# Kernel optimization log

Measured on AMD Instinct MI355X. Metric: run time of the kernel, lower is better.

Reference implementation:

```python
import jax, jax.numpy as jnp
import numpy as np

ENT_TYPES = 9
INNER_DIM = 64
BIG_NEG = 1e12


def _rope_tables(seq_len, dim, dtype):
    # sinusoidal_position_embedding: interleaved [sin, cos] of pos * 10000^(-2i/d)
    pos = jnp.arange(seq_len, dtype=jnp.float32)[:, None]            # [S,1]
    inv_freq = jnp.power(10000.0, -2.0 * jnp.arange(dim // 2, dtype=jnp.float32) / dim)
    ang = pos * inv_freq                                             # [S,D/2]
    emb = jnp.stack([jnp.sin(ang), jnp.cos(ang)], axis=-1).reshape(seq_len, dim)  # [S,D]
    cos_pos = jnp.repeat(emb[:, 1::2], 2, axis=-1).astype(dtype)     # [S,D]
    sin_pos = jnp.repeat(emb[:, ::2], 2, axis=-1).astype(dtype)      # [S,D]
    return cos_pos, sin_pos


def _rotate_half(x):
    # stack([-x[...,1::2], x[...,::2]], -1).reshape(x.shape)
    return jnp.stack([-x[..., 1::2], x[..., ::2]], axis=-1).reshape(x.shape)


def setup_inputs() -> dict:
    key = jax.random.key(0)
    k1, k2 = jax.random.split(key)
    B, S, H = 16, 512, 1024
    last_hidden_state = jax.random.normal(k1, (B, S, H), dtype=jnp.float32)
    padding_mask = jnp.ones((B, S), dtype=jnp.float32)
    W = jax.random.normal(k2, (H, ENT_TYPES * INNER_DIM * 2), dtype=jnp.float32) * (1.0 / np.sqrt(H))
    b = jnp.zeros((ENT_TYPES * INNER_DIM * 2,), dtype=jnp.float32)
    return {"last_hidden_state": last_hidden_state, "padding_mask": padding_mask, "W": W, "b": b}


def reference(last_hidden_state, padding_mask, W, b):
    B, S, _ = last_hidden_state.shape
    H, D = ENT_TYPES, INNER_DIM
    out = last_hidden_state @ W + b                 # [B,S,H*2D]
    out = out.reshape(B, S, H, 2 * D)
    qw, kw = out[..., :D], out[..., D:]             # [B,S,H,D]

    cos_pos, sin_pos = _rope_tables(S, D, qw.dtype)  # [S,D]
    cos_pos = cos_pos[None, :, None, :]
    sin_pos = sin_pos[None, :, None, :]
    qw = qw * cos_pos + _rotate_half(qw) * sin_pos
    kw = kw * cos_pos + _rotate_half(kw) * sin_pos

    logits = jnp.einsum('bmhd,bnhd->bhmn', qw, kw)   # [B,H,S,S]
    pad = padding_mask[:, None, None, :]             # mask over key dim
    logits = logits * pad - (1.0 - pad) * BIG_NEG
    tril = jnp.tril(jnp.ones((S, S), dtype=logits.dtype), -1)
    logits = logits - tril * BIG_NEG
    return logits / jnp.sqrt(jnp.asarray(D, dtype=logits.dtype))
```

## Files before the change

kernel.cpp:

```cpp
#include <hip/hip_runtime.h>

#define EN 9
#define DD 64
#define SS 512
#define NB 16
#define HH 1024
#define NOUT 1152

typedef short bf16x8 __attribute__((ext_vector_type(8)));
typedef short short4v __attribute__((ext_vector_type(4)));
typedef float f32x4 __attribute__((ext_vector_type(4)));

#define GPTR(p) ((const __attribute__((address_space(1))) void*)(p))
#define LPTR(p) ((__attribute__((address_space(3))) void*)(p))

__device__ inline unsigned short f2bf(float f) {
  unsigned int u = __float_as_uint(f);
  return (unsigned short)((u + 0x7FFFu + ((u >> 16) & 1u)) >> 16);
}

__global__ __launch_bounds__(256) void prep_kernel(
    const float* __restrict__ W, const float* __restrict__ X,
    unsigned short* __restrict__ Wt, unsigned short* __restrict__ Xb,
    float* __restrict__ ctab, float* __restrict__ stab) {
  if (blockIdx.x < 288u) {
    __shared__ float t[64][65];
    const int k0 = (blockIdx.x / 18) * 64;
    const int n0 = (blockIdx.x % 18) * 64;
    const int r = threadIdx.x >> 6;
    const int c = threadIdx.x & 63;
#pragma unroll
    for (int i = 0; i < 16; ++i) {
      const int kk = (i << 2) + r;
      t[kk][c] = W[(size_t)(k0 + kk) * NOUT + n0 + c];
    }
    __syncthreads();
#pragma unroll
    for (int i = 0; i < 16; ++i) {
      const int nn = (i << 2) + r;
      Wt[(size_t)(n0 + nn) * HH + k0 + c] = f2bf(t[c][nn]);
    }
  } else if (blockIdx.x < 304u) {
    const int bt = blockIdx.x - 288;
#pragma unroll
    for (int j = 0; j < 4; ++j) {
      const int id = bt * 1024 + j * 256 + threadIdx.x;
      const int s = id >> 5, i = id & 31;
      const float freq = expf(-(float)(2 * i) * (9.210340371976184f / 64.0f));
      const float ang = (float)s * freq;
      ctab[id] = cosf(ang);
      stab[id] = sinf(ang);
    }
  } else {
    const int bt = blockIdx.x - 304;
    const size_t base = (size_t)bt * 4096;
#pragma unroll
    for (int j = 0; j < 4; ++j) {
      const size_t idx = base + (size_t)((j << 8) + threadIdx.x) * 4;
      const float4 v = *(const float4*)(X + idx);
      short4v s4;
      s4[0] = (short)f2bf(v.x);
      s4[1] = (short)f2bf(v.y);
      s4[2] = (short)f2bf(v.z);
      s4[3] = (short)f2bf(v.w);
      *(short4v*)(Xb + idx) = s4;
    }
  }
}

__global__ __launch_bounds__(256, 2) void proj_rope_kernel(
    const unsigned short* __restrict__ Xb,
    const unsigned short* __restrict__ Wt, const float* __restrict__ bias,
    const float* __restrict__ ctab, const float* __restrict__ stab,
    unsigned short* __restrict__ QK) {
  __shared__ __align__(16) unsigned char sm[65536];
  const int tid = threadIdx.x;
  const int lane = tid & 63;
  const int wid = tid >> 6;
  const int wr = wid >> 1, wc = wid & 1;
  const int f = blockIdx.x;
  const int wkr = (f & 7) * 72 + (f >> 3);
  const int m0 = (wkr / 9) << 7;
  const int n0 = (wkr % 9) << 7;

  const int r_st = tid >> 3;
  const int cl_st = tid & 7;

  f32x4 acc[4][4];
#pragma unroll
  for (int i = 0; i < 4; ++i)
#pragma unroll
    for (int j = 0; j < 4; ++j) acc[i][j] = (f32x4){0.f, 0.f, 0.f, 0.f};

#define STAGE(BUF, KT)                                                        \
  {                                                                           \
    const int kt_ = (KT);                                                     \
    unsigned char* dst_ = sm + (BUF)*32768;                                   \
    _Pragma("unroll") for (int it = 0; it < 4; ++it) {                        \
      const int r_ = (it << 5) + r_st;                                        \
      const int cs_ = cl_st ^ (r_ & 7);                                       \
      __builtin_amdgcn_global_load_lds(                                       \
          GPTR(Xb + (size_t)(m0 + r_) * HH + kt_ + (cs_ << 3)),               \
          LPTR(dst_ + (((it << 8) + (wid << 6)) << 4)), 16, 0, 0);            \
      __builtin_amdgcn_global_load_lds(                                       \
          GPTR(Wt + (size_t)(n0 + r_) * HH + kt_ + (cs_ << 3)),               \
          LPTR(dst_ + 16384 + (((it << 8) + (wid << 6)) << 4)), 16, 0, 0);    \
    }                                                                         \
  }

#define COMPUTE(BUF)                                                          \
  {                                                                           \
    const unsigned char* smc_ = sm + (BUF)*32768;                             \
    _Pragma("unroll") for (int kb = 0; kb < 2; ++kb) {                        \
      bf16x8 af[4], bfr[4];                                                   \
      const int ca = (kb << 2) + (lane >> 4);                                 \
      _Pragma("unroll") for (int i = 0; i < 4; ++i) {                         \
        const int ra = (wr << 6) + (i << 4) + (lane & 15);                    \
        af[i] = *(const bf16x8*)(smc_ + (ra << 7) + ((ca ^ (ra & 7)) << 4));  \
        const int rb = (wc << 6) + (i << 4) + (lane & 15);                    \
        bfr[i] =                                                              \
            *(const bf16x8*)(smc_ + 16384 + (rb << 7) + ((ca ^ (rb & 7))      \
                                                         << 4));              \
      }                                                                       \
      _Pragma("unroll") for (int mi = 0; mi < 4; ++mi)                        \
          _Pragma("unroll") for (int ni = 0; ni < 4; ++ni) acc[mi][ni] =      \
          __builtin_amdgcn_mfma_f32_16x16x32_bf16(af[mi], bfr[ni],            \
                                                  acc[mi][ni], 0, 0, 0);      \
    }                                                                         \
  }

  STAGE(0, 0)
#pragma unroll 1
  for (int t = 0; t < 15; ++t) {
    STAGE((t + 1) & 1, (t + 1) << 6)
    asm volatile("s_waitcnt vmcnt(8)" ::: "memory");
    __builtin_amdgcn_s_barrier();
    __builtin_amdgcn_sched_barrier(0);
    COMPUTE(t & 1)
    __builtin_amdgcn_sched_barrier(0);
    __builtin_amdgcn_s_barrier();
  }
  asm volatile("s_waitcnt vmcnt(0)" ::: "memory");
  __builtin_amdgcn_s_barrier();
  __builtin_amdgcn_sched_barrier(0);
  COMPUTE(1)

#pragma unroll
  for (int mi = 0; mi < 4; ++mi) {
#pragma unroll
    for (int ni = 0; ni < 4; ++ni) {
      const int n = n0 + (wc << 6) + (ni << 4) + (lane & 15);
      const float bn = bias[n];
      const int h = n >> 7, t = (n >> 6) & 1, d = n & 63;
      const int i2 = d >> 1;
      const bool ev = (d & 1) == 0;
#pragma unroll
      for (int r = 0; r < 4; ++r) {
        const int m = m0 + (wr << 6) + (mi << 4) + ((lane >> 4) << 2) + r;
        const int s = m & (SS - 1);
        const int bb = m >> 9;
        const float v = acc[mi][ni][r] + bn;
        const float p = __shfl_xor(v, 1);
        const float cs = ctab[(s << 5) + i2];
        const float sn = stab[(s << 5) + i2];
        const float o = ev ? (v * cs - p * sn) : (v * cs + p * sn);
        QK[((((size_t)bb * EN + h) * 2 + t) * SS + s) * DD + d] = f2bf(o);
      }
    }
  }
}

__global__ __launch_bounds__(256, 4) void logits_kernel(
    const unsigned short* __restrict__ QK, const float* __restrict__ pmask,
    float* __restrict__ out) {
  __shared__ __align__(16) unsigned char sm[32768];
  const int tid = threadIdx.x;
  const int lane = tid & 63;
  const int wid = tid >> 6;
  const int wr = wid >> 1, wc = wid & 1;
  const int f = blockIdx.x;
  const int wkr = (f & 7) * 288 + (f >> 3);
  const int bh = wkr >> 4;
  const int bb = bh / EN;
  const int tm = (wkr >> 2) & 3, tn = wkr & 3;
  const int mq0 = tm << 7, nk0 = tn << 7;
  const unsigned short* Qb = QK + (size_t)bh * 2 * SS * DD;
  const unsigned short* Kb = Qb + SS * DD;

#pragma unroll
  for (int it = 0; it < 4; ++it) {
    const int q = it * 256 + tid;
    const int r = q >> 3, cl = q & 7;
    const int cs = cl ^ (r & 7);
    __builtin_amdgcn_global_load_lds(
        GPTR(Qb + (size_t)(mq0 + r) * DD + (cs << 3)),
        LPTR(sm + ((it * 256 + wid * 64) << 4)), 16, 0, 0);
    __builtin_amdgcn_global_load_lds(
        GPTR(Kb + (size_t)(nk0 + r) * DD + (cs << 3)),
        LPTR(sm + 16384 + ((it * 256 + wid * 64) << 4)), 16, 0, 0);
  }
  __syncthreads();

  f32x4 acc[4][4];
#pragma unroll
  for (int i = 0; i < 4; ++i)
#pragma unroll
    for (int j = 0; j < 4; ++j) acc[i][j] = (f32x4){0.f, 0.f, 0.f, 0.f};

#pragma unroll
  for (int kb = 0; kb < 2; ++kb) {
    bf16x8 af[4], bfr[4];
    const int ca = (kb << 2) + (lane >> 4);
#pragma unroll
    for (int i = 0; i < 4; ++i) {
      const int ra = (wr << 6) + (i << 4) + (lane & 15);
      af[i] = *(const bf16x8*)(sm + (ra << 7) + ((ca ^ (ra & 7)) << 4));
      const int rb = (wc << 6) + (i << 4) + (lane & 15);
      bfr[i] =
          *(const bf16x8*)(sm + 16384 + (rb << 7) + ((ca ^ (rb & 7)) << 4));
    }
#pragma unroll
    for (int mi = 0; mi < 4; ++mi)
#pragma unroll
      for (int ni = 0; ni < 4; ++ni)
        acc[mi][ni] = __builtin_amdgcn_mfma_f32_16x16x32_bf16(
            af[mi], bfr[ni], acc[mi][ni], 0, 0, 0);
  }

#pragma unroll
  for (int mi = 0; mi < 4; ++mi) {
#pragma unroll
    for (int ni = 0; ni < 4; ++ni) {
      const int n = nk0 + (wc << 6) + (ni << 4) + (lane & 15);
      const float pd = pmask[bb * SS + n];
      const float sub = (1.0f - pd) * 1e12f;
#pragma unroll
      for (int r = 0; r < 4; ++r) {
        const int m = mq0 + (wr << 6) + (mi << 4) + ((lane >> 4) << 2) + r;
        float v = acc[mi][ni][r] * pd - sub;
        if (m > n) v -= 1e12f;
        out[((size_t)bh * SS + m) * SS + n] = v * 0.125f;
      }
    }
  }
}

extern "C" void kernel_launch(void* const* d_in, const int* in_sizes, int n_in,
                              void* d_out, int out_size, void* d_ws,
                              size_t ws_size, hipStream_t stream) {
  const float* X = (const float*)d_in[0];
  const float* pm = (const float*)d_in[1];
  const float* W = (const float*)d_in[2];
  const float* bias = (const float*)d_in[3];
  float* out = (float*)d_out;
  unsigned char* ws = (unsigned char*)d_ws;
  unsigned short* QK = (unsigned short*)ws;
  unsigned short* Wt = (unsigned short*)(ws + 18874368);
  float* ctab = (float*)(ws + 21233664);
  float* stab = (float*)(ws + 21299200);
  unsigned short* Xb = (unsigned short*)(ws + 21364736);

  prep_kernel<<<dim3(2352), dim3(256), 0, stream>>>(W, X, Wt, Xb, ctab, stab);
  proj_rope_kernel<<<dim3(576), dim3(256), 0, stream>>>(Xb, Wt, bias, ctab,
                                                        stab, QK);
  logits_kernel<<<dim3(2304), dim3(256), 0, stream>>>(QK, pm, out);
}
```

Before: 71.84 us.

## Switch projection GEMM inputs from bf16 to fp8 with pre-swizzled layout

The prep kernel now converts X and W to fp8 (packed via cvt_pk_fp8) instead of bf16 and writes them in an XOR-swizzled layout. The projection GEMM then streams half the bytes, uses fp8 MFMA instructions, halves its LDS footprint to allow four blocks per CU, and raises wave priority during compute. The aim is to cut memory traffic and conversion cost in the prep and GEMM stages. It adds substantial precision loss in the projection, with a risk of accuracy tolerance failures.

```diff
diff --git a/kernel.cpp b/kernel.cpp
--- a/kernel.cpp
+++ b/kernel.cpp
@@ -3,12 +3,9 @@
 #define EN 9
 #define DD 64
 #define SS 512
-#define NB 16
 #define HH 1024
 #define NOUT 1152
 
-typedef short bf16x8 __attribute__((ext_vector_type(8)));
-typedef short short4v __attribute__((ext_vector_type(4)));
 typedef float f32x4 __attribute__((ext_vector_type(4)));
 
 #define GPTR(p) ((const __attribute__((address_space(1))) void*)(p))
@@ -19,9 +16,15 @@
   return (unsigned short)((u + 0x7FFFu + ((u >> 16) & 1u)) >> 16);
 }
 
+__device__ inline int pk4_fp8(float a, float b, float c, float d) {
+  int v = __builtin_amdgcn_cvt_pk_fp8_f32(a, b, 0, false);
+  v = __builtin_amdgcn_cvt_pk_fp8_f32(c, d, v, true);
+  return v;
+}
+
 __global__ __launch_bounds__(256) void prep_kernel(
     const float* __restrict__ W, const float* __restrict__ X,
-    unsigned short* __restrict__ Wt, unsigned short* __restrict__ Xb,
+    unsigned char* __restrict__ Wf8, unsigned char* __restrict__ Xf8,
     float* __restrict__ ctab, float* __restrict__ stab) {
   if (blockIdx.x < 288u) {
     __shared__ float t[64][65];
@@ -36,9 +39,18 @@
     }
     __syncthreads();
 #pragma unroll
-    for (int i = 0; i < 16; ++i) {
-      const int nn = (i << 2) + r;
-      Wt[(size_t)(n0 + nn) * HH + k0 + c] = f2bf(t[c][nn]);
+    for (int i = 0; i < 2; ++i) {
+      const int p = (i << 8) + threadIdx.x;
+      const int n = p >> 3, cc = p & 7;
+      const int kk = cc << 3;
+      const int lo = pk4_fp8(t[kk][n], t[kk + 1][n], t[kk + 2][n], t[kk + 3][n]);
+      const int hi =
+          pk4_fp8(t[kk + 4][n], t[kk + 5][n], t[kk + 6][n], t[kk + 7][n]);
+      const int gn = n0 + n;
+      int2 v;
+      v.x = lo;
+      v.y = hi;
+      *(int2*)(Wf8 + (size_t)gn * HH + k0 + ((cc ^ (gn & 7)) << 3)) = v;
     }
   } else if (blockIdx.x < 304u) {
     const int bt = blockIdx.x - 288;
@@ -53,27 +65,26 @@
     }
   } else {
     const int bt = blockIdx.x - 304;
-    const size_t base = (size_t)bt * 4096;
 #pragma unroll
     for (int j = 0; j < 4; ++j) {
-      const size_t idx = base + (size_t)((j << 8) + threadIdx.x) * 4;
-      const float4 v = *(const float4*)(X + idx);
-      short4v s4;
-      s4[0] = (short)f2bf(v.x);
-      s4[1] = (short)f2bf(v.y);
-      s4[2] = (short)f2bf(v.z);
-      s4[3] = (short)f2bf(v.w);
-      *(short4v*)(Xb + idx) = s4;
-    }
-  }
-}
-
-__global__ __launch_bounds__(256, 2) void proj_rope_kernel(
-    const unsigned short* __restrict__ Xb,
-    const unsigned short* __restrict__ Wt, const float* __restrict__ bias,
-    const float* __restrict__ ctab, const float* __restrict__ stab,
-    unsigned short* __restrict__ QK) {
-  __shared__ __align__(16) unsigned char sm[65536];
+      const int C = bt * 1024 + (j << 8) + threadIdx.x;
+      const int row = C >> 7, c = C & 127;
+      const float4 v0 = *(const float4*)(X + (size_t)C * 8);
+      const float4 v1 = *(const float4*)(X + (size_t)C * 8 + 4);
+      int2 v;
+      v.x = pk4_fp8(v0.x, v0.y, v0.z, v0.w);
+      v.y = pk4_fp8(v1.x, v1.y, v1.z, v1.w);
+      *(int2*)(Xf8 + (size_t)row * HH + ((c >> 3) << 6) +
+               (((c ^ row) & 7) << 3)) = v;
+    }
+  }
+}
+
+__global__ __launch_bounds__(256, 4) void proj_rope_kernel(
+    const unsigned char* __restrict__ Xf8, const unsigned char* __restrict__ Wf8,
+    const float* __restrict__ bias, const float* __restrict__ ctab,
+    const float* __restrict__ stab, unsigned short* __restrict__ QK) {
+  __shared__ __align__(16) unsigned char sm[32768];
   const int tid = threadIdx.x;
   const int lane = tid & 63;
   const int wid = tid >> 6;
@@ -83,57 +94,55 @@
   const int m0 = (wkr / 9) << 7;
   const int n0 = (wkr % 9) << 7;
 
-  const int r_st = tid >> 3;
-  const int cl_st = tid & 7;
-
   f32x4 acc[4][4];
 #pragma unroll
   for (int i = 0; i < 4; ++i)
 #pragma unroll
     for (int j = 0; j < 4; ++j) acc[i][j] = (f32x4){0.f, 0.f, 0.f, 0.f};
 
-#define STAGE(BUF, KT)                                                        \
-  {                                                                           \
-    const int kt_ = (KT);                                                     \
-    unsigned char* dst_ = sm + (BUF)*32768;                                   \
-    _Pragma("unroll") for (int it = 0; it < 4; ++it) {                        \
-      const int r_ = (it << 5) + r_st;                                        \
-      const int cs_ = cl_st ^ (r_ & 7);                                       \
-      __builtin_amdgcn_global_load_lds(                                       \
-          GPTR(Xb + (size_t)(m0 + r_) * HH + kt_ + (cs_ << 3)),               \
-          LPTR(dst_ + (((it << 8) + (wid << 6)) << 4)), 16, 0, 0);            \
-      __builtin_amdgcn_global_load_lds(                                       \
-          GPTR(Wt + (size_t)(n0 + r_) * HH + kt_ + (cs_ << 3)),               \
-          LPTR(dst_ + 16384 + (((it << 8) + (wid << 6)) << 4)), 16, 0, 0);    \
-    }                                                                         \
-  }
-
-#define COMPUTE(BUF)                                                          \
-  {                                                                           \
-    const unsigned char* smc_ = sm + (BUF)*32768;                             \
-    _Pragma("unroll") for (int kb = 0; kb < 2; ++kb) {                        \
-      bf16x8 af[4], bfr[4];                                                   \
-      const int ca = (kb << 2) + (lane >> 4);                                 \
-      _Pragma("unroll") for (int i = 0; i < 4; ++i) {                         \
-        const int ra = (wr << 6) + (i << 4) + (lane & 15);                    \
-        af[i] = *(const bf16x8*)(smc_ + (ra << 7) + ((ca ^ (ra & 7)) << 4));  \
-        const int rb = (wc << 6) + (i << 4) + (lane & 15);                    \
-        bfr[i] =                                                              \
-            *(const bf16x8*)(smc_ + 16384 + (rb << 7) + ((ca ^ (rb & 7))      \
-                                                         << 4));              \
-      }                                                                       \
-      _Pragma("unroll") for (int mi = 0; mi < 4; ++mi)                        \
-          _Pragma("unroll") for (int ni = 0; ni < 4; ++ni) acc[mi][ni] =      \
-          __builtin_amdgcn_mfma_f32_16x16x32_bf16(af[mi], bfr[ni],            \
-                                                  acc[mi][ni], 0, 0, 0);      \
-    }                                                                         \
+#define STAGE(BUF, KT)                                                       \
+  {                                                                          \
+    const int kt_ = (KT);                                                    \
+    unsigned char* dst_ = sm + (BUF)*16384;                                  \
+    _Pragma("unroll") for (int it = 0; it < 2; ++it) {                       \
+      const int u_ = (it << 8) + tid;                                        \
+      const int r_ = u_ >> 2, g_ = u_ & 3;                                   \
+      __builtin_amdgcn_global_load_lds(                                      \
+          GPTR(Xf8 + (size_t)(m0 + r_) * HH + kt_ + (g_ << 4)),              \
+          LPTR(dst_ + (((it << 8) + (wid << 6)) << 4)), 16, 0, 0);           \
+      __builtin_amdgcn_global_load_lds(                                      \
+          GPTR(Wf8 + (size_t)(n0 + r_) * HH + kt_ + (g_ << 4)),              \
+          LPTR(dst_ + 8192 + (((it << 8) + (wid << 6)) << 4)), 16, 0, 0);    \
+    }                                                                        \
+  }
+
+#define COMPUTE(BUF)                                                         \
+  {                                                                          \
+    const unsigned char* smc_ = sm + (BUF)*16384;                            \
+    __builtin_amdgcn_s_setprio(1);                                           \
+    _Pragma("unroll") for (int kb = 0; kb < 2; ++kb) {                       \
+      long aL[4], bL[4];                                                     \
+      const int c8 = (kb << 2) + (lane >> 4);                                \
+      _Pragma("unroll") for (int i = 0; i < 4; ++i) {                        \
+        const int ra = (wr << 6) + (i << 4) + (lane & 15);                   \
+        aL[i] = *(const long*)(smc_ + (ra << 6) + (((c8 ^ ra) & 7) << 3));   \
+        const int rb = (wc << 6) + (i << 4) + (lane & 15);                   \
+        bL[i] = *(const long*)(smc_ + 8192 + (rb << 6) +                     \
+                               (((c8 ^ rb) & 7) << 3));                      \
+      }                                                                      \
+      _Pragma("unroll") for (int mi = 0; mi < 4; ++mi)                       \
+          _Pragma("unroll") for (int ni = 0; ni < 4; ++ni) acc[mi][ni] =     \
+          __builtin_amdgcn_mfma_f32_16x16x32_fp8_fp8(aL[mi], bL[ni],         \
+                                                     acc[mi][ni], 0, 0, 0);  \
+    }                                                                        \
+    __builtin_amdgcn_s_setprio(0);                                           \
   }
 
   STAGE(0, 0)
 #pragma unroll 1
   for (int t = 0; t < 15; ++t) {
     STAGE((t + 1) & 1, (t + 1) << 6)
-    asm volatile("s_waitcnt vmcnt(8)" ::: "memory");
+    asm volatile("s_waitcnt vmcnt(4)" ::: "memory");
     __builtin_amdgcn_s_barrier();
     __builtin_amdgcn_sched_barrier(0);
     COMPUTE(t & 1)
@@ -207,6 +216,7 @@
 #pragma unroll
     for (int j = 0; j < 4; ++j) acc[i][j] = (f32x4){0.f, 0.f, 0.f, 0.f};
 
+  typedef short bf16x8 __attribute__((ext_vector_type(8)));
 #pragma unroll
   for (int kb = 0; kb < 2; ++kb) {
     bf16x8 af[4], bfr[4];
@@ -255,13 +265,13 @@
   float* out = (float*)d_out;
   unsigned char* ws = (unsigned char*)d_ws;
   unsigned short* QK = (unsigned short*)ws;
-  unsigned short* Wt = (unsigned short*)(ws + 18874368);
-  float* ctab = (float*)(ws + 21233664);
-  float* stab = (float*)(ws + 21299200);
-  unsigned short* Xb = (unsigned short*)(ws + 21364736);
-
-  prep_kernel<<<dim3(2352), dim3(256), 0, stream>>>(W, X, Wt, Xb, ctab, stab);
-  proj_rope_kernel<<<dim3(576), dim3(256), 0, stream>>>(Xb, Wt, bias, ctab,
+  unsigned char* Wf8 = ws + 18874368;
+  float* ctab = (float*)(ws + 20054016);
+  float* stab = (float*)(ws + 20119552);
+  unsigned char* Xf8 = ws + 20185088;
+
+  prep_kernel<<<dim3(1328), dim3(256), 0, stream>>>(W, X, Wf8, Xf8, ctab, stab);
+  proj_rope_kernel<<<dim3(576), dim3(256), 0, stream>>>(Xf8, Wf8, bias, ctab,
                                                         stab, QK);
   logits_kernel<<<dim3(2304), dim3(256), 0, stream>>>(QK, pm, out);
 }
```

Measured after the change: 62.95 us. 1.14x faster.
